# Optimization experiments

Hardware: AMD Instinct MI355X
Metric: run time of the kernel (lower is better)

Reference implementation:

```python
import math
import jax, jax.numpy as jnp
import numpy as np

WS = 8   # window_size
SS = 4   # shift_size
HEADS = 8
C = 256
B = 8
HH = 128
WW = 128


def _cpb_table_np(ws):
    # relative coords table: [(2ws-1)*(2ws-1), 2], log-spaced
    ch = np.arange(-(ws - 1), ws, dtype=np.float32)
    cw = np.arange(-(ws - 1), ws, dtype=np.float32)
    gh, gw = np.meshgrid(ch, cw, indexing='ij')
    t = np.stack([gh, gw], axis=-1).reshape(-1, 2)
    t = t / float(ws - 1)
    t = t * 8.0
    t = np.sign(t) * np.log2(np.abs(t) + 1.0) / math.log2(8)
    return t.astype(np.float32)


def _rel_pos_index_np(ws):
    ch = np.arange(ws)
    cw = np.arange(ws)
    gh, gw = np.meshgrid(ch, cw, indexing='ij')
    cf = np.stack([gh.reshape(-1), gw.reshape(-1)])  # [2, N]
    rel = cf[:, :, None] - cf[:, None, :]            # [2, N, N]
    rel = rel.transpose(1, 2, 0).astype(np.int64)
    rel[:, :, 0] += ws - 1
    rel[:, :, 1] += ws - 1
    rel[:, :, 0] *= 2 * ws - 1
    return rel.sum(-1)  # [N, N]


def _shift_mask_np(H, W, ws, ss):
    img = np.zeros((H, W), dtype=np.float32)
    cnt = 0
    for hs in (slice(0, -ws), slice(-ws, -ss), slice(-ss, None)):
        for wsl in (slice(0, -ws), slice(-ws, -ss), slice(-ss, None)):
            img[hs, wsl] = cnt
            cnt += 1
    nH, nW = H // ws, W // ws
    mw = img.reshape(nH, ws, nW, ws).transpose(0, 2, 1, 3).reshape(-1, ws * ws)  # [nWin, N]
    diff = mw[:, None, :] - mw[:, :, None]
    return np.where(diff != 0, -100.0, 0.0).astype(np.float32)  # [nWin, N, N]


def setup_inputs() -> dict:
    key = jax.random.key(0)
    ks = jax.random.split(key, 6)
    return {
        'x': jax.random.normal(ks[0], (B, HH * WW, C), dtype=jnp.float32),
        'qkv_w': jax.random.normal(ks[1], (3 * C, C), dtype=jnp.float32) * 0.02,
        'q_bias': jnp.zeros((C,), dtype=jnp.float32),
        'v_bias': jnp.zeros((C,), dtype=jnp.float32),
        'logit_scale': jnp.log(10.0 * jnp.ones((HEADS, 1, 1), dtype=jnp.float32)),
        'cpb_w1': jax.random.normal(ks[2], (512, 2), dtype=jnp.float32) * 0.02,
        'cpb_b1': jnp.zeros((512,), dtype=jnp.float32),
        'cpb_w2': jax.random.normal(ks[3], (HEADS, 512), dtype=jnp.float32) * 0.02,
        'proj_w': jax.random.normal(ks[4], (C, C), dtype=jnp.float32) * 0.02,
        'proj_b': jnp.zeros((C,), dtype=jnp.float32),
        'H': HH,
        'W': WW,
    }


def reference(x, qkv_w, q_bias, v_bias, logit_scale, cpb_w1, cpb_b1, cpb_w2,
              proj_w, proj_b, H, W):
    Bsz, L, Cd = x.shape
    heads = cpb_w2.shape[0]
    hd = Cd // heads
    N = WS * WS
    nH, nW = H // WS, W // WS
    nWin = nH * nW

    # shift + window partition
    xi = x.reshape(Bsz, H, W, Cd)
    xi = jnp.roll(xi, (-SS, -SS), axis=(1, 2))
    xw = xi.reshape(Bsz, nH, WS, nW, WS, Cd).transpose(0, 1, 3, 2, 4, 5)
    xw = xw.reshape(Bsz * nWin, N, Cd)  # [B_, N, C]

    # qkv with zeroed k-bias
    qkv_bias = jnp.concatenate([q_bias, jnp.zeros_like(v_bias), v_bias])
    qkv = xw @ qkv_w.T + qkv_bias  # [B_, N, 3C]
    qkv = qkv.reshape(Bsz * nWin, N, 3, heads, hd).transpose(2, 0, 3, 1, 4)
    q, k, v = qkv[0], qkv[1], qkv[2]  # [B_, h, N, d]

    # cosine attention
    qn = q / jnp.maximum(jnp.linalg.norm(q, axis=-1, keepdims=True), 1e-12)
    kn = k / jnp.maximum(jnp.linalg.norm(k, axis=-1, keepdims=True), 1e-12)
    attn = jnp.einsum('bhnd,bhmd->bhnm', qn, kn)
    scale = jnp.exp(jnp.minimum(logit_scale, math.log(1.0 / 0.01)))  # [h,1,1]
    attn = attn * scale[None]

    # log-CPB relative position bias
    table = jnp.asarray(_cpb_table_np(WS))                     # [(2W-1)^2, 2]
    hid = jax.nn.relu(table @ cpb_w1.T + cpb_b1)               # [T, 512]
    bias_table = hid @ cpb_w2.T                                # [T, h]
    rel_idx = jnp.asarray(_rel_pos_index_np(WS))               # [N, N]
    bias = bias_table[rel_idx.reshape(-1)].reshape(N, N, heads)
    bias = 16.0 * jax.nn.sigmoid(bias).transpose(2, 0, 1)      # [h, N, N]
    attn = attn + bias[None]

    # shift mask
    mask = jnp.asarray(_shift_mask_np(H, W, WS, SS))           # [nWin, N, N]
    attn = attn.reshape(Bsz, nWin, heads, N, N) + mask[None, :, None]
    attn = attn.reshape(Bsz * nWin, heads, N, N)

    attn = jax.nn.softmax(attn, axis=-1)
    out = jnp.einsum('bhnm,bhmd->bhnd', attn, v)
    out = out.transpose(0, 2, 1, 3).reshape(Bsz * nWin, N, Cd)
    out = out @ proj_w.T + proj_b

    # window reverse + unshift
    out = out.reshape(Bsz, nH, nW, WS, WS, Cd).transpose(0, 1, 3, 2, 4, 5)
    out = out.reshape(Bsz, H, W, Cd)
    out = jnp.roll(out, (SS, SS), axis=(1, 2))
    return out.reshape(Bsz, L, Cd)
```

## Files before the change

### kernel.cpp

```cpp
#include <hip/hip_runtime.h>
#include <cstdint>
#include <cstddef>

typedef short bf16x8 __attribute__((ext_vector_type(8)));
typedef float f32x4 __attribute__((ext_vector_type(4)));


#define WS_QKVW   0u
#define WS_PROJW  393216u
#define WS_QKVB   524288u
#define WS_SCALE  527360u
#define WS_BT     527392u
#define WS_BIAS   534592u

#define XS_US   0
#define QK_US   16896
#define VS_US   57856
#define SMEM_US 76288
#define SMEM_BYTES (SMEM_US * 2)

__device__ __forceinline__ unsigned short f2b(float f) {
  union { float f; unsigned int u; } v; v.f = f;
  return (unsigned short)((v.u + 0x7FFFu + ((v.u >> 16) & 1u)) >> 16);
}
__device__ __forceinline__ float b2f(unsigned short h) {
  union { unsigned int u; float f; } v; v.u = ((unsigned int)h) << 16;
  return v.f;
}


__global__ void prep_weights(const float* __restrict__ qkv_w,
                             const float* __restrict__ q_bias,
                             const float* __restrict__ v_bias,
                             const float* __restrict__ logit_scale,
                             const float* __restrict__ proj_w,
                             unsigned char* __restrict__ ws) {
  int gid = blockIdx.x * 256 + threadIdx.x;
  unsigned short* qw = (unsigned short*)(ws + WS_QKVW);
  unsigned short* pw = (unsigned short*)(ws + WS_PROJW);
  if (gid < 196608) qw[gid] = f2b(qkv_w[gid]);
  if (gid < 65536)  pw[gid] = f2b(proj_w[gid]);
  if (gid < 768) {
    float v = 0.f;
    if (gid < 256) v = q_bias[gid];
    else if (gid >= 512) v = v_bias[gid - 512];
    ((float*)(ws + WS_QKVB))[gid] = v;
  }
  if (gid < 8) {
    float ls = logit_scale[gid];
    ((float*)(ws + WS_SCALE))[gid] = __expf(fminf(ls, 4.605170185988091f));
  }
}

__global__ void prep_cpb(const float* __restrict__ w1, const float* __restrict__ b1,
                         const float* __restrict__ w2, unsigned char* __restrict__ ws) {
  __shared__ float hid[512];
  const int r = blockIdx.x;
  const int dh = r / 15, dw = r % 15;
  float t0 = ((float)(dh - 7)) / 7.0f * 8.0f;
  float t1 = ((float)(dw - 7)) / 7.0f * 8.0f;
  float a0 = log2f(fabsf(t0) + 1.0f) / 3.0f;
  float a1 = log2f(fabsf(t1) + 1.0f) / 3.0f;
  t0 = (t0 < 0.f) ? -a0 : a0;
  t1 = (t1 < 0.f) ? -a1 : a1;
  const int j = threadIdx.x;
  float h = t0 * w1[2 * j] + t1 * w1[2 * j + 1] + b1[j];
  hid[j] = fmaxf(h, 0.f);
  __syncthreads();
  const int wave = j >> 6, lane = j & 63;
  float p = 0.f;
  for (int jj = lane; jj < 512; jj += 64) p += hid[jj] * w2[wave * 512 + jj];
  #pragma unroll
  for (int off = 32; off > 0; off >>= 1) p += __shfl_down(p, off, 64);
  if (lane == 0) ((float*)(ws + WS_BT))[r * 8 + wave] = p;
}

__global__ void prep_bias(unsigned char* __restrict__ ws) {
  int u = blockIdx.x * 256 + threadIdx.x;
  int reg = u & 3;
  int lane = (u >> 2) & 63;
  int nt = (u >> 8) & 3;
  int mt = (u >> 10) & 3;
  int h = (u >> 12);
  int i = mt * 16 + (lane >> 4) * 4 + reg;
  int jx = nt * 16 + (lane & 15);
  int idx = ((i >> 3) - (jx >> 3) + 7) * 15 + ((i & 7) - (jx & 7) + 7);
  float xv = ((const float*)(ws + WS_BT))[idx * 8 + h];
  ((float*)(ws + WS_BIAS))[u] = 16.0f / (1.0f + __expf(-xv));
}


__launch_bounds__(512, 2)
__global__ void swin_main(const float* __restrict__ x,
                          const unsigned char* __restrict__ ws,
                          float* __restrict__ out,
                          const float* __restrict__ proj_b) {
  extern __shared__ unsigned short sm[];
  const int tid = threadIdx.x;
  const int wave = tid >> 6;
  const int lane = tid & 63;
  const int quad = lane >> 4;
  const int l15 = lane & 15;

  const int blk = blockIdx.x;
  const int b = blk >> 8;
  const int win = blk & 255;
  const int wr = win >> 4;
  const int wc = win & 15;

  const unsigned short* qkvw = (const unsigned short*)(ws + WS_QKVW);
  const unsigned short* projw = (const unsigned short*)(ws + WS_PROJW);
  const float* qkvb = (const float*)(ws + WS_QKVB);
  const float* scales = (const float*)(ws + WS_SCALE);
  const float* bias_sw = (const float*)(ws + WS_BIAS);

  {
    const int t = tid >> 3;
    const int cg = tid & 7;
    const int rw = t >> 3, cw = t & 7;
    const int gr = (wr * 8 + rw + 4) & 127;
    const int gc = (wc * 8 + cw + 4) & 127;
    const float* src = x + ((size_t)b * 16384 + gr * 128 + gc) * 256 + cg * 32;
    unsigned short* dst = sm + XS_US + t * 264 + cg * 32;
    #pragma unroll
    for (int kk = 0; kk < 4; ++kk) {
      f32x4 a = *(const f32x4*)(src + kk * 8);
      f32x4 c = *(const f32x4*)(src + kk * 8 + 4);
      union { bf16x8 v; unsigned short u[8]; } pk;
      #pragma unroll
      for (int e = 0; e < 4; ++e) { pk.u[e] = f2b(a[e]); pk.u[4 + e] = f2b(c[e]); }
      *(bf16x8*)(dst + kk * 8) = pk.v;
    }
  }
  __syncthreads();

  {
    f32x4 acc[4][6];
    #pragma unroll
    for (int mt = 0; mt < 4; ++mt)
      #pragma unroll
      for (int nt = 0; nt < 6; ++nt) acc[mt][nt] = f32x4{0.f, 0.f, 0.f, 0.f};
    const int ncol0 = wave * 96;
    for (int k0 = 0; k0 < 256; k0 += 32) {
      bf16x8 afr[4];
      #pragma unroll
      for (int mt = 0; mt < 4; ++mt)
        afr[mt] = *(const bf16x8*)(sm + XS_US + (mt * 16 + l15) * 264 + k0 + quad * 8);
      #pragma unroll
      for (int nt = 0; nt < 6; ++nt) {
        const int n = ncol0 + nt * 16 + l15;
        bf16x8 bfr = *(const bf16x8*)(qkvw + n * 256 + k0 + quad * 8);
        #pragma unroll
        for (int mt = 0; mt < 4; ++mt)
          acc[mt][nt] = __builtin_amdgcn_mfma_f32_16x16x32_bf16(afr[mt], bfr, acc[mt][nt], 0, 0, 0);
      }
    }
    #pragma unroll
    for (int nt = 0; nt < 6; ++nt) {
      const int n0 = ncol0 + nt * 16;
      const float bias = qkvb[n0 + l15];
      const int which = n0 >> 8;
      const int head = (n0 & 255) >> 5;
      const int chan = (n0 & 31) + l15;
      #pragma unroll
      for (int mt = 0; mt < 4; ++mt) {
        const int tok0 = mt * 16 + quad * 4;
        if (which == 2) {
          union { unsigned short u[4]; unsigned long long ll; } pk;
          #pragma unroll
          for (int r = 0; r < 4; ++r) pk.u[r] = f2b(acc[mt][nt][r] + bias);
          *(unsigned long long*)(sm + VS_US + head * 2304 + chan * 72 + tok0) = pk.ll;
        } else {
          unsigned short* q = sm + QK_US + head * 5120 + which * 2560 + chan;
          #pragma unroll
          for (int r = 0; r < 4; ++r) q[(tok0 + r) * 40] = f2b(acc[mt][nt][r] + bias);
        }
      }
    }
  }
  __syncthreads();

  {
    #pragma unroll
    for (int it = 0; it < 2; ++it) {
      const int task = tid + it * 512;
      const int isk = task >> 9;
      const int rem = task & 511;
      const int head = rem >> 6;
      const int tok = rem & 63;
      unsigned short* p = sm + QK_US + head * 5120 + isk * 2560 + tok * 40;
      float vals[32];
      float ss = 0.f;
      #pragma unroll
      for (int c8 = 0; c8 < 4; ++c8) {
        bf16x8 vv = *(const bf16x8*)(p + c8 * 8);
        #pragma unroll
        for (int e = 0; e < 8; ++e) {
          float f = b2f((unsigned short)vv[e]);
          vals[c8 * 8 + e] = f;
          ss += f * f;
        }
      }
      float inv = 1.0f / fmaxf(sqrtf(ss), 1e-12f);
      if (isk == 0) inv *= scales[head];
      #pragma unroll
      for (int c8 = 0; c8 < 4; ++c8) {
        union { bf16x8 v; unsigned short u[8]; } pk;
        #pragma unroll
        for (int e = 0; e < 8; ++e) pk.u[e] = f2b(vals[c8 * 8 + e] * inv);
        *(bf16x8*)(p + c8 * 8) = pk.v;
      }
    }
  }
  __syncthreads();

  float rinv[4][4];
  f32x4 o[4][2];
  {
    const int h = wave;
    const unsigned short* qb = sm + QK_US + h * 5120;
    const unsigned short* kb = qb + 2560;
    f32x4 s[4][4];
    bf16x8 aq[4];
    #pragma unroll
    for (int mt = 0; mt < 4; ++mt)
      aq[mt] = *(const bf16x8*)(qb + (mt * 16 + l15) * 40 + quad * 8);
    #pragma unroll
    for (int nt = 0; nt < 4; ++nt) {
      bf16x8 bk = *(const bf16x8*)(kb + (nt * 16 + l15) * 40 + quad * 8);
      #pragma unroll
      for (int mt = 0; mt < 4; ++mt)
        s[mt][nt] = __builtin_amdgcn_mfma_f32_16x16x32_bf16(aq[mt], bk, f32x4{0.f, 0.f, 0.f, 0.f}, 0, 0, 0);
    }
    const bool has_mask = (wr == 15) || (wc == 15);
    #pragma unroll
    for (int mt = 0; mt < 4; ++mt) {
      #pragma unroll
      for (int nt = 0; nt < 4; ++nt) {
        f32x4 bv = *(const f32x4*)(bias_sw + (size_t)(((h * 4 + mt) * 4 + nt) * 64 + lane) * 4);
        #pragma unroll
        for (int r = 0; r < 4; ++r) s[mt][nt][r] += bv[r];
        if (has_mask) {
          const int j = nt * 16 + l15;
          const int brj = (wr == 15) ? (((j >> 3) < 4) ? 1 : 2) : 0;
          const int bcj = (wc == 15) ? (((j & 7) < 4) ? 1 : 2) : 0;
          #pragma unroll
          for (int r = 0; r < 4; ++r) {
            const int i = mt * 16 + quad * 4 + r;
            const int bri = (wr == 15) ? (((i >> 3) < 4) ? 1 : 2) : 0;
            const int bci = (wc == 15) ? (((i & 7) < 4) ? 1 : 2) : 0;
            if (bri != brj || bci != bcj) s[mt][nt][r] -= 100.0f;
          }
        }
      }
    }
    #pragma unroll
    for (int mt = 0; mt < 4; ++mt) {
      #pragma unroll
      for (int r = 0; r < 4; ++r) {
        float m = fmaxf(fmaxf(s[mt][0][r], s[mt][1][r]), fmaxf(s[mt][2][r], s[mt][3][r]));
        #pragma unroll
        for (int off = 1; off < 16; off <<= 1) m = fmaxf(m, __shfl_xor(m, off, 64));
        float sum = 0.f;
        #pragma unroll
        for (int nt = 0; nt < 4; ++nt) {
          float p = __expf(s[mt][nt][r] - m);
          s[mt][nt][r] = p;
          sum += p;
        }
        #pragma unroll
        for (int off = 1; off < 16; off <<= 1) sum += __shfl_xor(sum, off, 64);
        rinv[mt][r] = 1.0f / sum;
      }
    }
    unsigned short* pbuf = sm + QK_US + h * 5120;
    #pragma unroll
    for (int mt = 0; mt < 4; ++mt) {
      #pragma unroll
      for (int r = 0; r < 4; ++r) {
        const int row = mt * 16 + quad * 4 + r;
        #pragma unroll
        for (int nt = 0; nt < 4; ++nt)
          pbuf[row * 72 + nt * 16 + l15] = f2b(s[mt][nt][r]);
      }
    }
    __syncthreads();
    #pragma unroll
    for (int mt = 0; mt < 4; ++mt)
      #pragma unroll
      for (int nc = 0; nc < 2; ++nc) o[mt][nc] = f32x4{0.f, 0.f, 0.f, 0.f};
    const unsigned short* vb = sm + VS_US + h * 2304;
    #pragma unroll
    for (int ks = 0; ks < 2; ++ks) {
      bf16x8 ap[4];
      #pragma unroll
      for (int mt = 0; mt < 4; ++mt)
        ap[mt] = *(const bf16x8*)(pbuf + (mt * 16 + l15) * 72 + ks * 32 + quad * 8);
      #pragma unroll
      for (int nc = 0; nc < 2; ++nc) {
        bf16x8 bv = *(const bf16x8*)(vb + (nc * 16 + l15) * 72 + ks * 32 + quad * 8);
        #pragma unroll
        for (int mt = 0; mt < 4; ++mt)
          o[mt][nc] = __builtin_amdgcn_mfma_f32_16x16x32_bf16(ap[mt], bv, o[mt][nc], 0, 0, 0);
      }
    }
    #pragma unroll
    for (int mt = 0; mt < 4; ++mt) {
      #pragma unroll
      for (int nc = 0; nc < 2; ++nc) {
        #pragma unroll
        for (int r = 0; r < 4; ++r) {
          const int tok = mt * 16 + quad * 4 + r;
          sm[XS_US + tok * 264 + h * 32 + nc * 16 + l15] = f2b(o[mt][nc][r] * rinv[mt][r]);
        }
      }
    }
  }
  __syncthreads();

  {
    f32x4 acc[4][2];
    #pragma unroll
    for (int mt = 0; mt < 4; ++mt)
      #pragma unroll
      for (int nt = 0; nt < 2; ++nt) acc[mt][nt] = f32x4{0.f, 0.f, 0.f, 0.f};
    const int ncol0 = wave * 32;
    for (int k0 = 0; k0 < 256; k0 += 32) {
      bf16x8 afr[4];
      #pragma unroll
      for (int mt = 0; mt < 4; ++mt)
        afr[mt] = *(const bf16x8*)(sm + XS_US + (mt * 16 + l15) * 264 + k0 + quad * 8);
      #pragma unroll
      for (int nt = 0; nt < 2; ++nt) {
        const int n = ncol0 + nt * 16 + l15;
        bf16x8 bfr = *(const bf16x8*)(projw + n * 256 + k0 + quad * 8);
        #pragma unroll
        for (int mt = 0; mt < 4; ++mt)
          acc[mt][nt] = __builtin_amdgcn_mfma_f32_16x16x32_bf16(afr[mt], bfr, acc[mt][nt], 0, 0, 0);
      }
    }
    #pragma unroll
    for (int nt = 0; nt < 2; ++nt) {
      const int col = ncol0 + nt * 16 + l15;
      const float pb = proj_b[col];
      #pragma unroll
      for (int mt = 0; mt < 4; ++mt) {
        #pragma unroll
        for (int r = 0; r < 4; ++r) {
          const int tok = mt * 16 + quad * 4 + r;
          const int rw = tok >> 3, cw = tok & 7;
          const int gr = (wr * 8 + rw + 4) & 127;
          const int gc = (wc * 8 + cw + 4) & 127;
          out[((size_t)b * 16384 + gr * 128 + gc) * 256 + col] = acc[mt][nt][r] + pb;
        }
      }
    }
  }
}


extern "C" void kernel_launch(void* const* d_in, const int* in_sizes, int n_in,
                              void* d_out, int out_size, void* d_ws, size_t ws_size,
                              hipStream_t stream) {
  const float* x           = (const float*)d_in[0];
  const float* qkv_w       = (const float*)d_in[1];
  const float* q_bias      = (const float*)d_in[2];
  const float* v_bias      = (const float*)d_in[3];
  const float* logit_scale = (const float*)d_in[4];
  const float* cpb_w1      = (const float*)d_in[5];
  const float* cpb_b1      = (const float*)d_in[6];
  const float* cpb_w2      = (const float*)d_in[7];
  const float* proj_w      = (const float*)d_in[8];
  const float* proj_b      = (const float*)d_in[9];
  unsigned char* ws = (unsigned char*)d_ws;
  float* out = (float*)d_out;

  prep_weights<<<768, 256, 0, stream>>>(qkv_w, q_bias, v_bias, logit_scale, proj_w, ws);
  prep_cpb<<<225, 512, 0, stream>>>(cpb_w1, cpb_b1, cpb_w2, ws);
  prep_bias<<<128, 256, 0, stream>>>(ws);

  (void)hipFuncSetAttribute((const void*)swin_main,
                            hipFuncAttributeMaxDynamicSharedMemorySize, SMEM_BYTES);
  swin_main<<<2048, 512, SMEM_BYTES, stream>>>(x, ws, out, proj_b);
}
```

Measured before the change: 491.0 us.

## Keep per-head Q/K/P in registers via transposed MFMA and lane shuffles

Each wave now computes its own head's Q and K projections in transposed form, normalizes them in registers, and repacks them into MFMA operand layout with cross-lane shuffles. Q/K no longer go through shared memory. Softmax probabilities are also kept in registers instead of a shared P buffer, and the bias table layout is transposed to match. This removes two block-wide barriers and cuts shared memory from ~150KB to ~70KB, and launch bounds are raised to 4 blocks per CU. The cost is more shuffle instructions and higher register pressure, which the tighter occupancy bound may force into spills.

```diff
diff --git a/kernel.cpp b/kernel.cpp
--- a/kernel.cpp
+++ b/kernel.cpp
@@ -14,18 +14,16 @@
 #define WS_BIAS   534592u
 
 #define XS_US   0
-#define QK_US   16896
-#define VS_US   57856
-#define SMEM_US 76288
+#define VT_US   16896
+#define SMEM_US 35328
 #define SMEM_BYTES (SMEM_US * 2)
 
 __device__ __forceinline__ unsigned short f2b(float f) {
   union { float f; unsigned int u; } v; v.f = f;
   return (unsigned short)((v.u + 0x7FFFu + ((v.u >> 16) & 1u)) >> 16);
 }
-__device__ __forceinline__ float b2f(unsigned short h) {
-  union { unsigned int u; float f; } v; v.u = ((unsigned int)h) << 16;
-  return v.f;
+__device__ __forceinline__ int pack2(float a, float b) {
+  return (int)(((unsigned)f2b(b) << 16) | (unsigned)f2b(a));
 }
 
 
@@ -77,20 +75,20 @@
 
 __global__ void prep_bias(unsigned char* __restrict__ ws) {
   int u = blockIdx.x * 256 + threadIdx.x;
-  int reg = u & 3;
+  int r = u & 3;
   int lane = (u >> 2) & 63;
-  int nt = (u >> 8) & 3;
-  int mt = (u >> 10) & 3;
+  int it = (u >> 8) & 3;
+  int jt = (u >> 10) & 3;
   int h = (u >> 12);
-  int i = mt * 16 + (lane >> 4) * 4 + reg;
-  int jx = nt * 16 + (lane & 15);
-  int idx = ((i >> 3) - (jx >> 3) + 7) * 15 + ((i & 7) - (jx & 7) + 7);
+  int i = it * 16 + (lane & 15);
+  int j = jt * 16 + (lane >> 4) * 4 + r;
+  int idx = ((i >> 3) - (j >> 3) + 7) * 15 + ((i & 7) - (j & 7) + 7);
   float xv = ((const float*)(ws + WS_BT))[idx * 8 + h];
   ((float*)(ws + WS_BIAS))[u] = 16.0f / (1.0f + __expf(-xv));
 }
 
 
-__launch_bounds__(512, 2)
+__launch_bounds__(512, 4)
 __global__ void swin_main(const float* __restrict__ x,
                           const unsigned char* __restrict__ ws,
                           float* __restrict__ out,
@@ -134,196 +132,224 @@
   }
   __syncthreads();
 
-  {
-    f32x4 acc[4][6];
+  const int h = wave;
+
+  f32x4 aQ[2][4], aK[2][4];
+  #pragma unroll
+  for (int ct = 0; ct < 2; ++ct)
+    #pragma unroll
+    for (int tt = 0; tt < 4; ++tt) { aQ[ct][tt] = f32x4{0,0,0,0}; aK[ct][tt] = f32x4{0,0,0,0}; }
+  for (int k0 = 0; k0 < 256; k0 += 32) {
+    bf16x8 xfr[4];
+    #pragma unroll
+    for (int tt = 0; tt < 4; ++tt)
+      xfr[tt] = *(const bf16x8*)(sm + XS_US + (tt * 16 + l15) * 264 + k0 + quad * 8);
+    bf16x8 wq[2], wk[2];
+    #pragma unroll
+    for (int ct = 0; ct < 2; ++ct) {
+      wq[ct] = *(const bf16x8*)(qkvw + (h * 32 + ct * 16 + l15) * 256 + k0 + quad * 8);
+      wk[ct] = *(const bf16x8*)(qkvw + (256 + h * 32 + ct * 16 + l15) * 256 + k0 + quad * 8);
+    }
+    #pragma unroll
+    for (int ct = 0; ct < 2; ++ct)
+      #pragma unroll
+      for (int tt = 0; tt < 4; ++tt) {
+        aQ[ct][tt] = __builtin_amdgcn_mfma_f32_16x16x32_bf16(wq[ct], xfr[tt], aQ[ct][tt], 0, 0, 0);
+        aK[ct][tt] = __builtin_amdgcn_mfma_f32_16x16x32_bf16(wk[ct], xfr[tt], aK[ct][tt], 0, 0, 0);
+      }
+  }
+  #pragma unroll
+  for (int ct = 0; ct < 2; ++ct)
+    #pragma unroll
+    for (int r = 0; r < 4; ++r) {
+      const float qb = qkvb[h * 32 + ct * 16 + quad * 4 + r];
+      #pragma unroll
+      for (int tt = 0; tt < 4; ++tt) aQ[ct][tt][r] += qb;
+    }
+  const float sc = scales[h];
+  int aqi[4][4], bki[4][4];
+  #pragma unroll
+  for (int tt = 0; tt < 4; ++tt) {
+    float ssq = 0.f, ssk = 0.f;
+    #pragma unroll
+    for (int ct = 0; ct < 2; ++ct)
+      #pragma unroll
+      for (int r = 0; r < 4; ++r) {
+        ssq += aQ[ct][tt][r] * aQ[ct][tt][r];
+        ssk += aK[ct][tt][r] * aK[ct][tt][r];
+      }
+    ssq += __shfl_xor(ssq, 16, 64); ssq += __shfl_xor(ssq, 32, 64);
+    ssk += __shfl_xor(ssk, 16, 64); ssk += __shfl_xor(ssk, 32, 64);
+    const float invq = sc / fmaxf(sqrtf(ssq), 1e-12f);
+    const float invk = 1.0f / fmaxf(sqrtf(ssk), 1e-12f);
+    int qp[2][2], kp[2][2];
+    #pragma unroll
+    for (int ct = 0; ct < 2; ++ct) {
+      qp[ct][0] = pack2(aQ[ct][tt][0] * invq, aQ[ct][tt][1] * invq);
+      qp[ct][1] = pack2(aQ[ct][tt][2] * invq, aQ[ct][tt][3] * invq);
+      kp[ct][0] = pack2(aK[ct][tt][0] * invk, aK[ct][tt][1] * invk);
+      kp[ct][1] = pack2(aK[ct][tt][2] * invk, aK[ct][tt][3] * invk);
+    }
+    #pragma unroll
+    for (int di = 0; di < 4; ++di) {
+      const int srcl = ((quad & 1) * 2 + (di >> 1)) * 16 + l15;
+      int a0 = __shfl(qp[0][di & 1], srcl, 64);
+      int a1 = __shfl(qp[1][di & 1], srcl, 64);
+      aqi[tt][di] = (quad >= 2) ? a1 : a0;
+      int b0 = __shfl(kp[0][di & 1], srcl, 64);
+      int b1 = __shfl(kp[1][di & 1], srcl, 64);
+      bki[tt][di] = (quad >= 2) ? b1 : b0;
+    }
+  }
+
+  {
+    f32x4 aV[4][2];
     #pragma unroll
     for (int mt = 0; mt < 4; ++mt)
       #pragma unroll
-      for (int nt = 0; nt < 6; ++nt) acc[mt][nt] = f32x4{0.f, 0.f, 0.f, 0.f};
-    const int ncol0 = wave * 96;
+      for (int nt = 0; nt < 2; ++nt) aV[mt][nt] = f32x4{0,0,0,0};
     for (int k0 = 0; k0 < 256; k0 += 32) {
-      bf16x8 afr[4];
+      bf16x8 xfr[4];
       #pragma unroll
       for (int mt = 0; mt < 4; ++mt)
-        afr[mt] = *(const bf16x8*)(sm + XS_US + (mt * 16 + l15) * 264 + k0 + quad * 8);
-      #pragma unroll
-      for (int nt = 0; nt < 6; ++nt) {
-        const int n = ncol0 + nt * 16 + l15;
-        bf16x8 bfr = *(const bf16x8*)(qkvw + n * 256 + k0 + quad * 8);
+        xfr[mt] = *(const bf16x8*)(sm + XS_US + (mt * 16 + l15) * 264 + k0 + quad * 8);
+      #pragma unroll
+      for (int nt = 0; nt < 2; ++nt) {
+        bf16x8 wv = *(const bf16x8*)(qkvw + (512 + h * 32 + nt * 16 + l15) * 256 + k0 + quad * 8);
         #pragma unroll
         for (int mt = 0; mt < 4; ++mt)
-          acc[mt][nt] = __builtin_amdgcn_mfma_f32_16x16x32_bf16(afr[mt], bfr, acc[mt][nt], 0, 0, 0);
-      }
-    }
-    #pragma unroll
-    for (int nt = 0; nt < 6; ++nt) {
-      const int n0 = ncol0 + nt * 16;
-      const float bias = qkvb[n0 + l15];
-      const int which = n0 >> 8;
-      const int head = (n0 & 255) >> 5;
-      const int chan = (n0 & 31) + l15;
+          aV[mt][nt] = __builtin_amdgcn_mfma_f32_16x16x32_bf16(xfr[mt], wv, aV[mt][nt], 0, 0, 0);
+      }
+    }
+    #pragma unroll
+    for (int nt = 0; nt < 2; ++nt) {
+      const float vb = qkvb[512 + h * 32 + nt * 16 + l15];
       #pragma unroll
       for (int mt = 0; mt < 4; ++mt) {
-        const int tok0 = mt * 16 + quad * 4;
-        if (which == 2) {
-          union { unsigned short u[4]; unsigned long long ll; } pk;
-          #pragma unroll
-          for (int r = 0; r < 4; ++r) pk.u[r] = f2b(acc[mt][nt][r] + bias);
-          *(unsigned long long*)(sm + VS_US + head * 2304 + chan * 72 + tok0) = pk.ll;
-        } else {
-          unsigned short* q = sm + QK_US + head * 5120 + which * 2560 + chan;
-          #pragma unroll
-          for (int r = 0; r < 4; ++r) q[(tok0 + r) * 40] = f2b(acc[mt][nt][r] + bias);
-        }
-      }
-    }
-  }
-  __syncthreads();
-
-  {
-    #pragma unroll
-    for (int it = 0; it < 2; ++it) {
-      const int task = tid + it * 512;
-      const int isk = task >> 9;
-      const int rem = task & 511;
-      const int head = rem >> 6;
-      const int tok = rem & 63;
-      unsigned short* p = sm + QK_US + head * 5120 + isk * 2560 + tok * 40;
-      float vals[32];
-      float ss = 0.f;
-      #pragma unroll
-      for (int c8 = 0; c8 < 4; ++c8) {
-        bf16x8 vv = *(const bf16x8*)(p + c8 * 8);
-        #pragma unroll
-        for (int e = 0; e < 8; ++e) {
-          float f = b2f((unsigned short)vv[e]);
-          vals[c8 * 8 + e] = f;
-          ss += f * f;
-        }
-      }
-      float inv = 1.0f / fmaxf(sqrtf(ss), 1e-12f);
-      if (isk == 0) inv *= scales[head];
-      #pragma unroll
-      for (int c8 = 0; c8 < 4; ++c8) {
-        union { bf16x8 v; unsigned short u[8]; } pk;
-        #pragma unroll
-        for (int e = 0; e < 8; ++e) pk.u[e] = f2b(vals[c8 * 8 + e] * inv);
-        *(bf16x8*)(p + c8 * 8) = pk.v;
-      }
-    }
-  }
-  __syncthreads();
-
-  float rinv[4][4];
-  f32x4 o[4][2];
-  {
-    const int h = wave;
-    const unsigned short* qb = sm + QK_US + h * 5120;
-    const unsigned short* kb = qb + 2560;
-    f32x4 s[4][4];
-    bf16x8 aq[4];
-    #pragma unroll
-    for (int mt = 0; mt < 4; ++mt)
-      aq[mt] = *(const bf16x8*)(qb + (mt * 16 + l15) * 40 + quad * 8);
-    #pragma unroll
-    for (int nt = 0; nt < 4; ++nt) {
-      bf16x8 bk = *(const bf16x8*)(kb + (nt * 16 + l15) * 40 + quad * 8);
-      #pragma unroll
-      for (int mt = 0; mt < 4; ++mt)
-        s[mt][nt] = __builtin_amdgcn_mfma_f32_16x16x32_bf16(aq[mt], bk, f32x4{0.f, 0.f, 0.f, 0.f}, 0, 0, 0);
-    }
+        int w0 = pack2(aV[mt][nt][0] + vb, aV[mt][nt][1] + vb);
+        int w1 = pack2(aV[mt][nt][2] + vb, aV[mt][nt][3] + vb);
+        int2* dst = (int2*)(sm + VT_US + h * 2304 + (nt * 16 + l15) * 72 + mt * 16 + quad * 4);
+        *dst = int2{w0, w1};
+      }
+    }
+  }
+
+  union { int i[4]; bf16x8 v; } fa, fb;
+  f32x4 S[4][4];
+  {
+    bf16x8 aq[4], bk[4];
+    #pragma unroll
+    for (int tt = 0; tt < 4; ++tt) {
+      #pragma unroll
+      for (int di = 0; di < 4; ++di) { fa.i[di] = aqi[tt][di]; fb.i[di] = bki[tt][di]; }
+      aq[tt] = fa.v; bk[tt] = fb.v;
+    }
+    #pragma unroll
+    for (int jt = 0; jt < 4; ++jt)
+      #pragma unroll
+      for (int it = 0; it < 4; ++it)
+        S[jt][it] = __builtin_amdgcn_mfma_f32_16x16x32_bf16(bk[jt], aq[it], f32x4{0,0,0,0}, 0, 0, 0);
+  }
+  {
     const bool has_mask = (wr == 15) || (wc == 15);
     #pragma unroll
-    for (int mt = 0; mt < 4; ++mt) {
-      #pragma unroll
-      for (int nt = 0; nt < 4; ++nt) {
-        f32x4 bv = *(const f32x4*)(bias_sw + (size_t)(((h * 4 + mt) * 4 + nt) * 64 + lane) * 4);
-        #pragma unroll
-        for (int r = 0; r < 4; ++r) s[mt][nt][r] += bv[r];
+    for (int jt = 0; jt < 4; ++jt)
+      #pragma unroll
+      for (int it = 0; it < 4; ++it) {
+        f32x4 bv = *(const f32x4*)(bias_sw + (size_t)(((h * 4 + jt) * 4 + it) * 64 + lane) * 4);
+        #pragma unroll
+        for (int r = 0; r < 4; ++r) S[jt][it][r] += bv[r];
         if (has_mask) {
-          const int j = nt * 16 + l15;
-          const int brj = (wr == 15) ? (((j >> 3) < 4) ? 1 : 2) : 0;
-          const int bcj = (wc == 15) ? (((j & 7) < 4) ? 1 : 2) : 0;
+          const int i = it * 16 + l15;
+          const int bri = (wr == 15) ? (((i >> 3) < 4) ? 1 : 2) : 0;
+          const int bci = (wc == 15) ? (((i & 7) < 4) ? 1 : 2) : 0;
           #pragma unroll
           for (int r = 0; r < 4; ++r) {
-            const int i = mt * 16 + quad * 4 + r;
-            const int bri = (wr == 15) ? (((i >> 3) < 4) ? 1 : 2) : 0;
-            const int bci = (wc == 15) ? (((i & 7) < 4) ? 1 : 2) : 0;
-            if (bri != brj || bci != bcj) s[mt][nt][r] -= 100.0f;
+            const int j = jt * 16 + quad * 4 + r;
+            const int brj = (wr == 15) ? (((j >> 3) < 4) ? 1 : 2) : 0;
+            const int bcj = (wc == 15) ? (((j & 7) < 4) ? 1 : 2) : 0;
+            if (bri != brj || bci != bcj) S[jt][it][r] -= 100.0f;
           }
         }
       }
-    }
-    #pragma unroll
-    for (int mt = 0; mt < 4; ++mt) {
-      #pragma unroll
-      for (int r = 0; r < 4; ++r) {
-        float m = fmaxf(fmaxf(s[mt][0][r], s[mt][1][r]), fmaxf(s[mt][2][r], s[mt][3][r]));
-        #pragma unroll
-        for (int off = 1; off < 16; off <<= 1) m = fmaxf(m, __shfl_xor(m, off, 64));
-        float sum = 0.f;
-        #pragma unroll
-        for (int nt = 0; nt < 4; ++nt) {
-          float p = __expf(s[mt][nt][r] - m);
-          s[mt][nt][r] = p;
-          sum += p;
+  }
+  int api[4][2][4];
+  {
+    #pragma unroll
+    for (int it = 0; it < 4; ++it) {
+      float m = -1e30f;
+      #pragma unroll
+      for (int jt = 0; jt < 4; ++jt)
+        #pragma unroll
+        for (int r = 0; r < 4; ++r) m = fmaxf(m, S[jt][it][r]);
+      m = fmaxf(m, __shfl_xor(m, 16, 64));
+      m = fmaxf(m, __shfl_xor(m, 32, 64));
+      float sum = 0.f;
+      #pragma unroll
+      for (int jt = 0; jt < 4; ++jt)
+        #pragma unroll
+        for (int r = 0; r < 4; ++r) { float p = __expf(S[jt][it][r] - m); S[jt][it][r] = p; sum += p; }
+      sum += __shfl_xor(sum, 16, 64);
+      sum += __shfl_xor(sum, 32, 64);
+      const float rinv = 1.0f / sum;
+      int sp[4][2];
+      #pragma unroll
+      for (int jt = 0; jt < 4; ++jt) {
+        sp[jt][0] = pack2(S[jt][it][0] * rinv, S[jt][it][1] * rinv);
+        sp[jt][1] = pack2(S[jt][it][2] * rinv, S[jt][it][3] * rinv);
+      }
+      #pragma unroll
+      for (int ks = 0; ks < 2; ++ks)
+        #pragma unroll
+        for (int di = 0; di < 4; ++di) {
+          const int srcl = ((quad & 1) * 2 + (di >> 1)) * 16 + l15;
+          int c0 = __shfl(sp[ks * 2][di & 1], srcl, 64);
+          int c1 = __shfl(sp[ks * 2 + 1][di & 1], srcl, 64);
+          api[it][ks][di] = (quad >= 2) ? c1 : c0;
         }
-        #pragma unroll
-        for (int off = 1; off < 16; off <<= 1) sum += __shfl_xor(sum, off, 64);
-        rinv[mt][r] = 1.0f / sum;
-      }
-    }
-    unsigned short* pbuf = sm + QK_US + h * 5120;
-    #pragma unroll
-    for (int mt = 0; mt < 4; ++mt) {
-      #pragma unroll
-      for (int r = 0; r < 4; ++r) {
-        const int row = mt * 16 + quad * 4 + r;
-        #pragma unroll
-        for (int nt = 0; nt < 4; ++nt)
-          pbuf[row * 72 + nt * 16 + l15] = f2b(s[mt][nt][r]);
-      }
-    }
-    __syncthreads();
+    }
+  }
+  __syncthreads();
+
+  {
+    f32x4 aO[4][2];
+    #pragma unroll
+    for (int it = 0; it < 4; ++it)
+      #pragma unroll
+      for (int c2 = 0; c2 < 2; ++c2) aO[it][c2] = f32x4{0,0,0,0};
+    #pragma unroll
+    for (int ks = 0; ks < 2; ++ks) {
+      bf16x8 vfr[2];
+      #pragma unroll
+      for (int c2 = 0; c2 < 2; ++c2)
+        vfr[c2] = *(const bf16x8*)(sm + VT_US + h * 2304 + (c2 * 16 + l15) * 72 + ks * 32 + quad * 8);
+      #pragma unroll
+      for (int it = 0; it < 4; ++it) {
+        #pragma unroll
+        for (int di = 0; di < 4; ++di) fa.i[di] = api[it][ks][di];
+        #pragma unroll
+        for (int c2 = 0; c2 < 2; ++c2)
+          aO[it][c2] = __builtin_amdgcn_mfma_f32_16x16x32_bf16(fa.v, vfr[c2], aO[it][c2], 0, 0, 0);
+      }
+    }
+    #pragma unroll
+    for (int it = 0; it < 4; ++it)
+      #pragma unroll
+      for (int c2 = 0; c2 < 2; ++c2)
+        #pragma unroll
+        for (int r = 0; r < 4; ++r) {
+          const int tok = it * 16 + quad * 4 + r;
+          sm[XS_US + tok * 264 + h * 32 + c2 * 16 + l15] = f2b(aO[it][c2][r]);
+        }
+  }
+  __syncthreads();
+
+  {
+    f32x4 acc[4][2];
     #pragma unroll
     for (int mt = 0; mt < 4; ++mt)
       #pragma unroll
-      for (int nc = 0; nc < 2; ++nc) o[mt][nc] = f32x4{0.f, 0.f, 0.f, 0.f};
-    const unsigned short* vb = sm + VS_US + h * 2304;
-    #pragma unroll
-    for (int ks = 0; ks < 2; ++ks) {
-      bf16x8 ap[4];
-      #pragma unroll
-      for (int mt = 0; mt < 4; ++mt)
-        ap[mt] = *(const bf16x8*)(pbuf + (mt * 16 + l15) * 72 + ks * 32 + quad * 8);
-      #pragma unroll
-      for (int nc = 0; nc < 2; ++nc) {
-        bf16x8 bv = *(const bf16x8*)(vb + (nc * 16 + l15) * 72 + ks * 32 + quad * 8);
-        #pragma unroll
-        for (int mt = 0; mt < 4; ++mt)
-          o[mt][nc] = __builtin_amdgcn_mfma_f32_16x16x32_bf16(ap[mt], bv, o[mt][nc], 0, 0, 0);
-      }
-    }
-    #pragma unroll
-    for (int mt = 0; mt < 4; ++mt) {
-      #pragma unroll
-      for (int nc = 0; nc < 2; ++nc) {
-        #pragma unroll
-        for (int r = 0; r < 4; ++r) {
-          const int tok = mt * 16 + quad * 4 + r;
-          sm[XS_US + tok * 264 + h * 32 + nc * 16 + l15] = f2b(o[mt][nc][r] * rinv[mt][r]);
-        }
-      }
-    }
-  }
-  __syncthreads();
-
-  {
-    f32x4 acc[4][2];
-    #pragma unroll
-    for (int mt = 0; mt < 4; ++mt)
-      #pragma unroll
-      for (int nt = 0; nt < 2; ++nt) acc[mt][nt] = f32x4{0.f, 0.f, 0.f, 0.f};
+      for (int nt = 0; nt < 2; ++nt) acc[mt][nt] = f32x4{0,0,0,0};
     const int ncol0 = wave * 32;
     for (int k0 = 0; k0 < 256; k0 += 32) {
       bf16x8 afr[4];
@@ -332,8 +358,7 @@
         afr[mt] = *(const bf16x8*)(sm + XS_US + (mt * 16 + l15) * 264 + k0 + quad * 8);
       #pragma unroll
       for (int nt = 0; nt < 2; ++nt) {
-        const int n = ncol0 + nt * 16 + l15;
-        bf16x8 bfr = *(const bf16x8*)(projw + n * 256 + k0 + quad * 8);
+        bf16x8 bfr = *(const bf16x8*)(projw + (ncol0 + nt * 16 + l15) * 256 + k0 + quad * 8);
         #pragma unroll
         for (int mt = 0; mt < 4; ++mt)
           acc[mt][nt] = __builtin_amdgcn_mfma_f32_16x16x32_bf16(afr[mt], bfr, acc[mt][nt], 0, 0, 0);
```

Result: slower. 536.4 us (+9.2%).
